# Kernel tuning notes

Hardware: AMD Instinct MI355X
Metric: run time of the kernel (lower is better)

## Reference

```python
import jax, jax.numpy as jnp
import numpy as np

T = 5          # Newton-Schulz iterations
EPS = 1e-05


def reference(X):
    # X: (B, C, L); training-mode IterNorm whitening with num_groups=1
    B, C, L = X.shape
    x = jnp.transpose(X, (1, 0, 2)).reshape(C, -1)        # (d, m)
    d, m = x.shape
    mean = jnp.mean(x, axis=-1, keepdims=True)
    xc = x - mean                                         # (d, m)
    I = jnp.eye(d, dtype=X.dtype)
    Sigma = I * EPS + (xc @ xc.T) * (1.0 / m)             # (d, d)
    rTr = 1.0 / jnp.trace(Sigma)                          # scalar
    Sigma_N = Sigma * rTr
    P = I
    for _ in range(T):
        P = 1.5 * P - 0.5 * (P @ P @ P) @ Sigma_N
    wm = P * jnp.sqrt(rTr)                                # whitening matrix
    xn = wm @ xc                                          # (d, m)
    Xn = jnp.transpose(xn.reshape(C, B, L), (1, 0, 2))
    return Xn


def setup_inputs() -> dict:
    key = jax.random.key(0)
    X = jax.random.normal(key, (32, 64, 8192), dtype=jnp.float32)
    return {"X": X}
```

## Files before the change

kernel.cpp:

```cpp
#include <hip/hip_runtime.h>
#include <math.h>

#define L_DIM   8192
#define NCH     64
#define M_TOT_F 262144.0f
#define EPS_F   1e-5f

typedef float f32x4 __attribute__((ext_vector_type(4)));
typedef short bf16x8 __attribute__((ext_vector_type(8)));

union U8 { unsigned u[4]; bf16x8 v; };

__device__ __forceinline__ void cvt2(float f0, float f1, unsigned& h, unsigned& l) {
    unsigned u0 = __float_as_uint(f0), u1 = __float_as_uint(f1);
    h = (u0 >> 16) | (u1 & 0xFFFF0000u);
    float r0 = f0 - __uint_as_float(u0 & 0xFFFF0000u);
    float r1 = f1 - __uint_as_float(u1 & 0xFFFF0000u);
    l = (__float_as_uint(r0) >> 16) | (__float_as_uint(r1) & 0xFFFF0000u);
}

__device__ __forceinline__ void cvt8(const float* p, bf16x8& hi, bf16x8& lo) {
    float4 f0 = *(const float4*)p;
    float4 f1 = *(const float4*)(p + 4);
    U8 H, L;
    cvt2(f0.x, f0.y, H.u[0], L.u[0]);
    cvt2(f0.z, f0.w, H.u[1], L.u[1]);
    cvt2(f1.x, f1.y, H.u[2], L.u[2]);
    cvt2(f1.z, f1.w, H.u[3], L.u[3]);
    hi = H.v; lo = L.v;
}

__device__ __forceinline__ f32x4 mfma16(bf16x8 a, bf16x8 b, f32x4 c) {
    return __builtin_amdgcn_mfma_f32_16x16x32_bf16(a, b, c, 0, 0, 0);
}

__device__ __forceinline__ f32x4 fzero() {
    f32x4 z; z[0] = 0.f; z[1] = 0.f; z[2] = 0.f; z[3] = 0.f; return z;
}

#define GTPB 8
__global__ __launch_bounds__(256) void gram_kernel(const float* __restrict__ X,
                                                   float* __restrict__ P) {
    __shared__ __align__(16) unsigned short hplane[64 * 72];
    __shared__ __align__(16) unsigned short lplane[64 * 72];
    const int tid  = threadIdx.x;
    const int w    = tid >> 6;
    const int lane = tid & 63;
    const int m    = lane & 15;
    const int q    = lane >> 4;
    const int lrow = tid >> 2;
    const int lq16 = (tid & 3) << 4;

    f32x4 acc1[4], acc2[4];
#pragma unroll
    for (int nb = 0; nb < 4; ++nb) { acc1[nb] = fzero(); acc2[nb] = fzero(); }
    float sacc = 0.f;

    const int tile0 = blockIdx.x * GTPB;
    float4 v[4];
    {
        int t = tile0;
        const float* src = X + ((size_t)((t >> 7) * NCH + lrow)) * L_DIM + ((t & 127) << 6) + lq16;
#pragma unroll
        for (int i = 0; i < 4; ++i) v[i] = ((const float4*)src)[i];
    }

    for (int t = 0; t < GTPB; ++t) {
#pragma unroll
        for (int i = 0; i < 4; ++i) sacc += v[i].x + v[i].y + v[i].z + v[i].w;
        __syncthreads();
#pragma unroll
        for (int i = 0; i < 4; ++i) {
            unsigned h0, l0, h1, l1;
            cvt2(v[i].x, v[i].y, h0, l0);
            cvt2(v[i].z, v[i].w, h1, l1);
            uint2 hh; hh.x = h0; hh.y = h1;
            uint2 ll; ll.x = l0; ll.y = l1;
            *(uint2*)&hplane[lrow * 72 + lq16 + 4 * i] = hh;
            *(uint2*)&lplane[lrow * 72 + lq16 + 4 * i] = ll;
        }
        __syncthreads();
        if (t + 1 < GTPB) {
            int tn = tile0 + t + 1;
            const float* src = X + ((size_t)((tn >> 7) * NCH + lrow)) * L_DIM + ((tn & 127) << 6) + lq16;
#pragma unroll
            for (int i = 0; i < 4; ++i) v[i] = ((const float4*)src)[i];
        }
#pragma unroll
        for (int k0 = 0; k0 < 64; k0 += 32) {
            bf16x8 a = *(const bf16x8*)&hplane[(16 * w + m) * 72 + k0 + 8 * q];
#pragma unroll
            for (int nb = 0; nb < 4; ++nb) {
                bf16x8 bh = *(const bf16x8*)&hplane[(16 * nb + m) * 72 + k0 + 8 * q];
                bf16x8 bl = *(const bf16x8*)&lplane[(16 * nb + m) * 72 + k0 + 8 * q];
                acc1[nb] = mfma16(a, bh, acc1[nb]);
                acc2[nb] = mfma16(a, bl, acc2[nb]);
            }
        }
    }

    float* base = P + (size_t)blockIdx.x * 8256;
#pragma unroll
    for (int nb = 0; nb < 4; ++nb)
#pragma unroll
        for (int r = 0; r < 4; ++r) {
            int grow = 16 * w + 4 * q + r;
            int gcol = 16 * nb + m;
            base[grow * 64 + gcol]        = acc1[nb][r];
            base[4096 + grow * 64 + gcol] = acc2[nb][r];
        }
    sacc += __shfl_xor(sacc, 1);
    sacc += __shfl_xor(sacc, 2);
    if ((tid & 3) == 0) base[8192 + lrow] = sacc;
}

__global__ __launch_bounds__(256) void reduce_kernel(const float* __restrict__ P,
                                                     float* __restrict__ ws) {
    const int tid = threadIdx.x;
    const int w = tid >> 6, lane = tid & 63;
    const int e0 = blockIdx.x * 64;
    float a = 0.f;
#pragma unroll 8
    for (int i = 0; i < 128; ++i)
        a += P[(size_t)(w * 128 + i) * 8256 + e0 + lane];
    __shared__ float red[4][64];
    red[w][lane] = a;
    __syncthreads();
    if (w == 0)
        ws[e0 + lane] = red[0][lane] + red[1][lane] + red[2][lane] + red[3][lane];
}

__device__ __forceinline__ void mm_sym(float* __restrict__ D, const float* __restrict__ A,
                                       const float* __restrict__ B, int w, int m, int q) {
    f32x4 acc[4];
#pragma unroll
    for (int nb = 0; nb < 4; ++nb) acc[nb] = fzero();
#pragma unroll
    for (int k0 = 0; k0 < 64; k0 += 32) {
        bf16x8 ah, al;
        cvt8(&A[(16 * w + m) * 68 + k0 + 8 * q], ah, al);
#pragma unroll
        for (int nb = 0; nb < 4; ++nb) {
            bf16x8 bh, bl;
            cvt8(&B[(16 * nb + m) * 68 + k0 + 8 * q], bh, bl);
            acc[nb] = mfma16(ah, bh, acc[nb]);
            acc[nb] = mfma16(ah, bl, acc[nb]);
            acc[nb] = mfma16(al, bh, acc[nb]);
        }
    }
#pragma unroll
    for (int nb = 0; nb < 4; ++nb)
#pragma unroll
        for (int r = 0; r < 4; ++r)
            D[(16 * w + 4 * q + r) * 68 + 16 * nb + m] = acc[nb][r];
}

__global__ __launch_bounds__(256) void ns_kernel(float* __restrict__ ws) {
    __shared__ __align__(16) float S[64 * 68];
    __shared__ __align__(16) float Pm[64 * 68];
    __shared__ __align__(16) float T1[64 * 68];
    __shared__ __align__(16) float T2[64 * 68];
    __shared__ float mu[64];
    __shared__ float scal[2];

    const int tid = threadIdx.x;
    const int w = tid >> 6, lane = tid & 63;
    const int m = lane & 15, q = lane >> 4;
    const float inv_m = 1.0f / M_TOT_F;

    if (tid < 64) mu[tid] = ws[8192 + tid] * inv_m;
    __syncthreads();

    for (int e = tid; e < 4096; e += 256) {
        int i = e >> 6, j = e & 63;
        float g = (ws[e] + ws[4096 + e] + ws[4096 + (j << 6) + i]) * inv_m;
        S[i * 68 + j]  = g - mu[i] * mu[j] + ((i == j) ? EPS_F : 0.f);
        Pm[i * 68 + j] = (i == j) ? 1.f : 0.f;
    }
    __syncthreads();

    if (tid < 64) {
        float v = S[tid * 68 + tid];
#pragma unroll
        for (int off = 32; off >= 1; off >>= 1) v += __shfl_xor(v, off);
        if (tid == 0) { scal[0] = 1.0f / v; scal[1] = sqrtf(1.0f / v); }
    }
    __syncthreads();
    const float rTr = scal[0];
    for (int e = tid; e < 4096; e += 256) S[(e >> 6) * 68 + (e & 63)] *= rTr;
    __syncthreads();

    for (int it = 0; it < 5; ++it) {
        mm_sym(T1, Pm, Pm, w, m, q);
        __syncthreads();
        mm_sym(T2, T1, Pm, w, m, q);
        __syncthreads();
        f32x4 acc[4];
#pragma unroll
        for (int nb = 0; nb < 4; ++nb) acc[nb] = fzero();
#pragma unroll
        for (int k0 = 0; k0 < 64; k0 += 32) {
            bf16x8 ah, al;
            cvt8(&T2[(16 * w + m) * 68 + k0 + 8 * q], ah, al);
#pragma unroll
            for (int nb = 0; nb < 4; ++nb) {
                bf16x8 bh, bl;
                cvt8(&S[(16 * nb + m) * 68 + k0 + 8 * q], bh, bl);
                acc[nb] = mfma16(ah, bh, acc[nb]);
                acc[nb] = mfma16(ah, bl, acc[nb]);
                acc[nb] = mfma16(al, bh, acc[nb]);
            }
        }
#pragma unroll
        for (int nb = 0; nb < 4; ++nb)
#pragma unroll
            for (int r = 0; r < 4; ++r) {
                int idx = (16 * w + 4 * q + r) * 68 + 16 * nb + m;
                Pm[idx] = 1.5f * Pm[idx] - 0.5f * acc[nb][r];
            }
        __syncthreads();
    }

    const float s = scal[1];
    unsigned short* hp = (unsigned short*)ws;
    unsigned short* lp = hp + 4096;
    for (int e = tid; e < 4096; e += 256) {
        int i = e >> 6, j = e & 63;
        float v = Pm[i * 68 + j] * s;
        unsigned u = __float_as_uint(v);
        hp[e] = (unsigned short)(u >> 16);
        float r = v - __uint_as_float(u & 0xFFFF0000u);
        lp[e] = (unsigned short)(__float_as_uint(r) >> 16);
    }
    if (tid < 64) {
        float a = 0.f;
#pragma unroll 8
        for (int k = 0; k < 64; ++k) a += Pm[tid * 68 + k] * mu[k];
        ws[8256 + tid] = -a * s;
    }
}

#define ATPB 4
__global__ __launch_bounds__(256) void apply_kernel(const float* __restrict__ X,
                                                    float* __restrict__ Y,
                                                    const float* __restrict__ ws) {
    __shared__ __align__(16) unsigned short hplane[4096];
    __shared__ __align__(16) unsigned short lplane[4096];
    const int tid  = threadIdx.x;
    const int w    = tid >> 6;
    const int lane = tid & 63;
    const int m    = lane & 15;
    const int q    = lane >> 4;
    const int cp   = tid & 31;
    const int lg   = tid >> 5;

    const unsigned short* hp = (const unsigned short*)ws;
    const unsigned short* lp = hp + 4096;
    bf16x8 Ah[2], Al[2];
#pragma unroll
    for (int kk = 0; kk < 2; ++kk) {
        Ah[kk] = *(const bf16x8*)&hp[(16 * w + m) * 64 + 32 * kk + 8 * q];
        Al[kk] = *(const bf16x8*)&lp[(16 * w + m) * 64 + 32 * kk + 8 * q];
    }
    const float4 bias4 = *(const float4*)&ws[8256 + 16 * w + 4 * q];

    unsigned* hw = (unsigned*)hplane;
    unsigned* lw = (unsigned*)lplane;

    float4 va[2], vb[2];
    {
        int tile = blockIdx.x * ATPB;
        const float* xb = X + (size_t)(tile >> 7) * (NCH * L_DIM) + ((tile & 127) << 6)
                          + (size_t)(2 * cp) * L_DIM + 4 * lg;
#pragma unroll
        for (int s = 0; s < 2; ++s) {
            va[s] = *(const float4*)(xb + 32 * s);
            vb[s] = *(const float4*)(xb + 32 * s + L_DIM);
        }
    }

    for (int t = 0; t < ATPB; ++t) {
        int tile = blockIdx.x * ATPB + t;
        int bidx = tile >> 7;
        int l0   = (tile & 127) << 6;

        __syncthreads();
#pragma unroll
        for (int s = 0; s < 2; ++s) {
            float fa[4], fb[4];
            *(float4*)fa = va[s];
            *(float4*)fb = vb[s];
#pragma unroll
            for (int i = 0; i < 4; ++i) {
                int l = 4 * lg + 32 * s + i;
                unsigned h, lo2;
                cvt2(fa[i], fb[i], h, lo2);
                int widx = l * 32 + (((cp >> 2) ^ (l & 7)) << 2) + (cp & 3);
                hw[widx] = h;
                lw[widx] = lo2;
            }
        }
        __syncthreads();

        if (t + 1 < ATPB) {
            int tn = tile + 1;
            const float* xb = X + (size_t)(tn >> 7) * (NCH * L_DIM) + ((tn & 127) << 6)
                              + (size_t)(2 * cp) * L_DIM + 4 * lg;
#pragma unroll
            for (int s = 0; s < 2; ++s) {
                va[s] = *(const float4*)(xb + 32 * s);
                vb[s] = *(const float4*)(xb + 32 * s + L_DIM);
            }
        }

        f32x4 acc[4];
#pragma unroll
        for (int nb = 0; nb < 4; ++nb) {
            acc[nb][0] = bias4.x; acc[nb][1] = bias4.y;
            acc[nb][2] = bias4.z; acc[nb][3] = bias4.w;
        }
#pragma unroll
        for (int kk = 0; kk < 2; ++kk)
#pragma unroll
            for (int nb = 0; nb < 4; ++nb) {
                int l = 16 * nb + m;
                int saddr = l * 64 + ((((4 * kk + q) ^ (l & 7))) << 3);
                bf16x8 bh = *(const bf16x8*)&hplane[saddr];
                bf16x8 bl = *(const bf16x8*)&lplane[saddr];
                acc[nb] = mfma16(Ah[kk], bh, acc[nb]);
                acc[nb] = mfma16(Ah[kk], bl, acc[nb]);
                acc[nb] = mfma16(Al[kk], bh, acc[nb]);
            }

#pragma unroll
        for (int nb = 0; nb < 4; ++nb)
#pragma unroll
            for (int rr = 0; rr < 4; ++rr)
                Y[((size_t)bidx * NCH + 16 * w + 4 * q + rr) * L_DIM + l0 + 16 * nb + m] = acc[nb][rr];
    }
}

extern "C" void kernel_launch(void* const* d_in, const int* in_sizes, int n_in,
                              void* d_out, int out_size, void* d_ws, size_t ws_size,
                              hipStream_t stream) {
    const float* X = (const float*)d_in[0];
    float* Y  = (float*)d_out;
    float* ws = (float*)d_ws;
    float* scratch = (float*)d_out;

    hipLaunchKernelGGL(gram_kernel,   dim3(512),  dim3(256), 0, stream, X, scratch);
    hipLaunchKernelGGL(reduce_kernel, dim3(129),  dim3(256), 0, stream, scratch, ws);
    hipLaunchKernelGGL(ns_kernel,     dim3(1),    dim3(256), 0, stream, ws);
    hipLaunchKernelGGL(apply_kernel,  dim3(1024), dim3(256), 0, stream, X, Y, ws);
}
```

Measured before the change: 159.7 us.

## Double-buffer LDS tiles, store NS operands pre-split, peel first NS iteration, double gram grid

Gram and apply kernels now alternate between two LDS buffers, so one barrier per tile is dropped. The gram grid doubles with half the tiles per block, and the reduce kernel sums twice as many partials. The Newton-Schulz kernel keeps its matrices as pre-split bf16 hi/lo planes instead of re-splitting fp32 at every matmul. Its first iteration is computed analytically (P=I gives 1.5I-0.5S), leaving four matmul iterations. The costs are more LDS per block in gram/apply and a larger partial buffer to reduce.

```diff
diff --git a/kernel.cpp b/kernel.cpp
--- a/kernel.cpp
+++ b/kernel.cpp
@@ -19,15 +19,11 @@
     l = (__float_as_uint(r0) >> 16) | (__float_as_uint(r1) & 0xFFFF0000u);
 }
 
-__device__ __forceinline__ void cvt8(const float* p, bf16x8& hi, bf16x8& lo) {
-    float4 f0 = *(const float4*)p;
-    float4 f1 = *(const float4*)(p + 4);
-    U8 H, L;
-    cvt2(f0.x, f0.y, H.u[0], L.u[0]);
-    cvt2(f0.z, f0.w, H.u[1], L.u[1]);
-    cvt2(f1.x, f1.y, H.u[2], L.u[2]);
-    cvt2(f1.z, f1.w, H.u[3], L.u[3]);
-    hi = H.v; lo = L.v;
+__device__ __forceinline__ void split16(float v, unsigned short& h, unsigned short& l) {
+    unsigned u = __float_as_uint(v);
+    h = (unsigned short)(u >> 16);
+    float r = v - __uint_as_float(u & 0xFFFF0000u);
+    l = (unsigned short)(__float_as_uint(r) >> 16);
 }
 
 __device__ __forceinline__ f32x4 mfma16(bf16x8 a, bf16x8 b, f32x4 c) {
@@ -38,11 +34,11 @@
     f32x4 z; z[0] = 0.f; z[1] = 0.f; z[2] = 0.f; z[3] = 0.f; return z;
 }
 
-#define GTPB 8
+#define GTPB 4
 __global__ __launch_bounds__(256) void gram_kernel(const float* __restrict__ X,
                                                    float* __restrict__ P) {
-    __shared__ __align__(16) unsigned short hplane[64 * 72];
-    __shared__ __align__(16) unsigned short lplane[64 * 72];
+    __shared__ __align__(16) unsigned short hplane[2][64 * 72];
+    __shared__ __align__(16) unsigned short lplane[2][64 * 72];
     const int tid  = threadIdx.x;
     const int w    = tid >> 6;
     const int lane = tid & 63;
@@ -66,9 +62,9 @@
     }
 
     for (int t = 0; t < GTPB; ++t) {
+        const int p = t & 1;
 #pragma unroll
         for (int i = 0; i < 4; ++i) sacc += v[i].x + v[i].y + v[i].z + v[i].w;
-        __syncthreads();
 #pragma unroll
         for (int i = 0; i < 4; ++i) {
             unsigned h0, l0, h1, l1;
@@ -76,23 +72,23 @@
             cvt2(v[i].z, v[i].w, h1, l1);
             uint2 hh; hh.x = h0; hh.y = h1;
             uint2 ll; ll.x = l0; ll.y = l1;
-            *(uint2*)&hplane[lrow * 72 + lq16 + 4 * i] = hh;
-            *(uint2*)&lplane[lrow * 72 + lq16 + 4 * i] = ll;
-        }
-        __syncthreads();
+            *(uint2*)&hplane[p][lrow * 72 + lq16 + 4 * i] = hh;
+            *(uint2*)&lplane[p][lrow * 72 + lq16 + 4 * i] = ll;
+        }
         if (t + 1 < GTPB) {
             int tn = tile0 + t + 1;
             const float* src = X + ((size_t)((tn >> 7) * NCH + lrow)) * L_DIM + ((tn & 127) << 6) + lq16;
 #pragma unroll
             for (int i = 0; i < 4; ++i) v[i] = ((const float4*)src)[i];
         }
+        __syncthreads();
 #pragma unroll
         for (int k0 = 0; k0 < 64; k0 += 32) {
-            bf16x8 a = *(const bf16x8*)&hplane[(16 * w + m) * 72 + k0 + 8 * q];
+            bf16x8 a = *(const bf16x8*)&hplane[p][(16 * w + m) * 72 + k0 + 8 * q];
 #pragma unroll
             for (int nb = 0; nb < 4; ++nb) {
-                bf16x8 bh = *(const bf16x8*)&hplane[(16 * nb + m) * 72 + k0 + 8 * q];
-                bf16x8 bl = *(const bf16x8*)&lplane[(16 * nb + m) * 72 + k0 + 8 * q];
+                bf16x8 bh = *(const bf16x8*)&hplane[p][(16 * nb + m) * 72 + k0 + 8 * q];
+                bf16x8 bl = *(const bf16x8*)&lplane[p][(16 * nb + m) * 72 + k0 + 8 * q];
                 acc1[nb] = mfma16(a, bh, acc1[nb]);
                 acc2[nb] = mfma16(a, bl, acc2[nb]);
             }
@@ -121,8 +117,8 @@
     const int e0 = blockIdx.x * 64;
     float a = 0.f;
 #pragma unroll 8
-    for (int i = 0; i < 128; ++i)
-        a += P[(size_t)(w * 128 + i) * 8256 + e0 + lane];
+    for (int i = 0; i < 256; ++i)
+        a += P[(size_t)(w * 256 + i) * 8256 + e0 + lane];
     __shared__ float red[4][64];
     red[w][lane] = a;
     __syncthreads();
@@ -130,36 +126,56 @@
         ws[e0 + lane] = red[0][lane] + red[1][lane] + red[2][lane] + red[3][lane];
 }
 
-__device__ __forceinline__ void mm_sym(float* __restrict__ D, const float* __restrict__ A,
-                                       const float* __restrict__ B, int w, int m, int q) {
+__device__ __forceinline__ void mm_core(f32x4* acc,
+                                        const unsigned short* __restrict__ Xh,
+                                        const unsigned short* __restrict__ Xl,
+                                        const unsigned short* __restrict__ Yh,
+                                        const unsigned short* __restrict__ Yl,
+                                        int w, int m, int q) {
+#pragma unroll
+    for (int k0 = 0; k0 < 64; k0 += 32) {
+        bf16x8 xh = *(const bf16x8*)&Xh[(16 * w + m) * 72 + k0 + 8 * q];
+        bf16x8 xl = *(const bf16x8*)&Xl[(16 * w + m) * 72 + k0 + 8 * q];
+#pragma unroll
+        for (int nb = 0; nb < 4; ++nb) {
+            bf16x8 yh = *(const bf16x8*)&Yh[(16 * nb + m) * 72 + k0 + 8 * q];
+            bf16x8 yl = *(const bf16x8*)&Yl[(16 * nb + m) * 72 + k0 + 8 * q];
+            acc[nb] = mfma16(xh, yh, acc[nb]);
+            acc[nb] = mfma16(xh, yl, acc[nb]);
+            acc[nb] = mfma16(xl, yh, acc[nb]);
+        }
+    }
+}
+
+__device__ __forceinline__ void mm_pl(unsigned short* __restrict__ Dh,
+                                      unsigned short* __restrict__ Dl,
+                                      const unsigned short* __restrict__ Xh,
+                                      const unsigned short* __restrict__ Xl,
+                                      const unsigned short* __restrict__ Yh,
+                                      const unsigned short* __restrict__ Yl,
+                                      int w, int m, int q) {
     f32x4 acc[4];
 #pragma unroll
     for (int nb = 0; nb < 4; ++nb) acc[nb] = fzero();
-#pragma unroll
-    for (int k0 = 0; k0 < 64; k0 += 32) {
-        bf16x8 ah, al;
-        cvt8(&A[(16 * w + m) * 68 + k0 + 8 * q], ah, al);
-#pragma unroll
-        for (int nb = 0; nb < 4; ++nb) {
-            bf16x8 bh, bl;
-            cvt8(&B[(16 * nb + m) * 68 + k0 + 8 * q], bh, bl);
-            acc[nb] = mfma16(ah, bh, acc[nb]);
-            acc[nb] = mfma16(ah, bl, acc[nb]);
-            acc[nb] = mfma16(al, bh, acc[nb]);
-        }
-    }
+    mm_core(acc, Xh, Xl, Yh, Yl, w, m, q);
 #pragma unroll
     for (int nb = 0; nb < 4; ++nb)
 #pragma unroll
-        for (int r = 0; r < 4; ++r)
-            D[(16 * w + 4 * q + r) * 68 + 16 * nb + m] = acc[nb][r];
+        for (int r = 0; r < 4; ++r) {
+            int row = 16 * w + 4 * q + r, col = 16 * nb + m;
+            unsigned short h, l;
+            split16(acc[nb][r], h, l);
+            Dh[row * 72 + col] = h;
+            Dl[row * 72 + col] = l;
+        }
 }
 
 __global__ __launch_bounds__(256) void ns_kernel(float* __restrict__ ws) {
-    __shared__ __align__(16) float S[64 * 68];
-    __shared__ __align__(16) float Pm[64 * 68];
-    __shared__ __align__(16) float T1[64 * 68];
-    __shared__ __align__(16) float T2[64 * 68];
+    __shared__ __align__(16) float Pf[64 * 68];
+    __shared__ __align__(16) unsigned short Ph[64 * 72], Pl[64 * 72];
+    __shared__ __align__(16) unsigned short Sh[64 * 72], Sl[64 * 72];
+    __shared__ __align__(16) unsigned short T1h[64 * 72], T1l[64 * 72];
+    __shared__ __align__(16) unsigned short T2h[64 * 72], T2l[64 * 72];
     __shared__ float mu[64];
     __shared__ float scal[2];
 
@@ -174,49 +190,53 @@
     for (int e = tid; e < 4096; e += 256) {
         int i = e >> 6, j = e & 63;
         float g = (ws[e] + ws[4096 + e] + ws[4096 + (j << 6) + i]) * inv_m;
-        S[i * 68 + j]  = g - mu[i] * mu[j] + ((i == j) ? EPS_F : 0.f);
-        Pm[i * 68 + j] = (i == j) ? 1.f : 0.f;
+        Pf[i * 68 + j] = g - mu[i] * mu[j] + ((i == j) ? EPS_F : 0.f);
     }
     __syncthreads();
 
     if (tid < 64) {
-        float v = S[tid * 68 + tid];
+        float v = Pf[tid * 68 + tid];
 #pragma unroll
         for (int off = 32; off >= 1; off >>= 1) v += __shfl_xor(v, off);
         if (tid == 0) { scal[0] = 1.0f / v; scal[1] = sqrtf(1.0f / v); }
     }
     __syncthreads();
     const float rTr = scal[0];
-    for (int e = tid; e < 4096; e += 256) S[(e >> 6) * 68 + (e & 63)] *= rTr;
-    __syncthreads();
-
-    for (int it = 0; it < 5; ++it) {
-        mm_sym(T1, Pm, Pm, w, m, q);
-        __syncthreads();
-        mm_sym(T2, T1, Pm, w, m, q);
+
+    for (int e = tid; e < 4096; e += 256) {
+        int i = e >> 6, j = e & 63;
+        float sn = Pf[i * 68 + j] * rTr;
+        unsigned short h, l;
+        split16(sn, h, l);
+        Sh[i * 72 + j] = h; Sl[i * 72 + j] = l;
+        float pv = ((i == j) ? 1.5f : 0.f) - 0.5f * sn;
+        Pf[i * 68 + j] = pv;
+        split16(pv, h, l);
+        Ph[i * 72 + j] = h; Pl[i * 72 + j] = l;
+    }
+    __syncthreads();
+
+    for (int it = 0; it < 4; ++it) {
+        mm_pl(T1h, T1l, Ph, Pl, Ph, Pl, w, m, q);
+        __syncthreads();
+        mm_pl(T2h, T2l, T1h, T1l, Ph, Pl, w, m, q);
         __syncthreads();
         f32x4 acc[4];
 #pragma unroll
         for (int nb = 0; nb < 4; ++nb) acc[nb] = fzero();
-#pragma unroll
-        for (int k0 = 0; k0 < 64; k0 += 32) {
-            bf16x8 ah, al;
-            cvt8(&T2[(16 * w + m) * 68 + k0 + 8 * q], ah, al);
-#pragma unroll
-            for (int nb = 0; nb < 4; ++nb) {
-                bf16x8 bh, bl;
-                cvt8(&S[(16 * nb + m) * 68 + k0 + 8 * q], bh, bl);
-                acc[nb] = mfma16(ah, bh, acc[nb]);
-                acc[nb] = mfma16(ah, bl, acc[nb]);
-                acc[nb] = mfma16(al, bh, acc[nb]);
-            }
-        }
+        mm_core(acc, T2h, T2l, Sh, Sl, w, m, q);
 #pragma unroll
         for (int nb = 0; nb < 4; ++nb)
 #pragma unroll
             for (int r = 0; r < 4; ++r) {
-                int idx = (16 * w + 4 * q + r) * 68 + 16 * nb + m;
-                Pm[idx] = 1.5f * Pm[idx] - 0.5f * acc[nb][r];
+                int row = 16 * w + 4 * q + r, col = 16 * nb + m;
+                int idx = row * 68 + col;
+                float pv = 1.5f * Pf[idx] - 0.5f * acc[nb][r];
+                Pf[idx] = pv;
+                unsigned short h, l;
+                split16(pv, h, l);
+                Ph[row * 72 + col] = h;
+                Pl[row * 72 + col] = l;
             }
         __syncthreads();
     }
@@ -226,16 +246,16 @@
     unsigned short* lp = hp + 4096;
     for (int e = tid; e < 4096; e += 256) {
         int i = e >> 6, j = e & 63;
-        float v = Pm[i * 68 + j] * s;
-        unsigned u = __float_as_uint(v);
-        hp[e] = (unsigned short)(u >> 16);
-        float r = v - __uint_as_float(u & 0xFFFF0000u);
-        lp[e] = (unsigned short)(__float_as_uint(r) >> 16);
+        float v = Pf[i * 68 + j] * s;
+        unsigned short h, l;
+        split16(v, h, l);
+        hp[e] = h;
+        lp[e] = l;
     }
     if (tid < 64) {
         float a = 0.f;
 #pragma unroll 8
-        for (int k = 0; k < 64; ++k) a += Pm[tid * 68 + k] * mu[k];
+        for (int k = 0; k < 64; ++k) a += Pf[tid * 68 + k] * mu[k];
         ws[8256 + tid] = -a * s;
     }
 }
@@ -244,8 +264,8 @@
 __global__ __launch_bounds__(256) void apply_kernel(const float* __restrict__ X,
                                                     float* __restrict__ Y,
                                                     const float* __restrict__ ws) {
-    __shared__ __align__(16) unsigned short hplane[4096];
-    __shared__ __align__(16) unsigned short lplane[4096];
+    __shared__ __align__(16) unsigned short hplane[2][4096];
+    __shared__ __align__(16) unsigned short lplane[2][4096];
     const int tid  = threadIdx.x;
     const int w    = tid >> 6;
     const int lane = tid & 63;
@@ -264,9 +284,6 @@
     }
     const float4 bias4 = *(const float4*)&ws[8256 + 16 * w + 4 * q];
 
-    unsigned* hw = (unsigned*)hplane;
-    unsigned* lw = (unsigned*)lplane;
-
     float4 va[2], vb[2];
     {
         int tile = blockIdx.x * ATPB;
@@ -283,8 +300,10 @@
         int tile = blockIdx.x * ATPB + t;
         int bidx = tile >> 7;
         int l0   = (tile & 127) << 6;
-
-        __syncthreads();
+        const int p = t & 1;
+        unsigned* hw = (unsigned*)hplane[p];
+        unsigned* lw = (unsigned*)lplane[p];
+
 #pragma unroll
         for (int s = 0; s < 2; ++s) {
             float fa[4], fb[4];
@@ -300,7 +319,6 @@
                 lw[widx] = lo2;
             }
         }
-        __syncthreads();
 
         if (t + 1 < ATPB) {
             int tn = tile + 1;
@@ -312,6 +330,7 @@
                 vb[s] = *(const float4*)(xb + 32 * s + L_DIM);
             }
         }
+        __syncthreads();
 
         f32x4 acc[4];
 #pragma unroll
@@ -325,8 +344,8 @@
             for (int nb = 0; nb < 4; ++nb) {
                 int l = 16 * nb + m;
                 int saddr = l * 64 + ((((4 * kk + q) ^ (l & 7))) << 3);
-                bf16x8 bh = *(const bf16x8*)&hplane[saddr];
-                bf16x8 bl = *(const bf16x8*)&lplane[saddr];
+                bf16x8 bh = *(const bf16x8*)&hplane[p][saddr];
+                bf16x8 bl = *(const bf16x8*)&lplane[p][saddr];
                 acc[nb] = mfma16(Ah[kk], bh, acc[nb]);
                 acc[nb] = mfma16(Ah[kk], bl, acc[nb]);
                 acc[nb] = mfma16(Al[kk], bh, acc[nb]);
@@ -348,7 +367,7 @@
     float* ws = (float*)d_ws;
     float* scratch = (float*)d_out;
 
-    hipLaunchKernelGGL(gram_kernel,   dim3(512),  dim3(256), 0, stream, X, scratch);
+    hipLaunchKernelGGL(gram_kernel,   dim3(1024), dim3(256), 0, stream, X, scratch);
     hipLaunchKernelGGL(reduce_kernel, dim3(129),  dim3(256), 0, stream, scratch, ws);
     hipLaunchKernelGGL(ns_kernel,     dim3(1),    dim3(256), 0, stream, ws);
     hipLaunchKernelGGL(apply_kernel,  dim3(1024), dim3(256), 0, stream, X, Y, ws);
```

After: 156.3 us. 2.1% less time.
